# Kernel tuning notes

Measured on AMD Instinct MI355X. Metric: run time of the kernel, lower is better.

Reference implementation:

```python
import jax, jax.numpy as jnp
import numpy as np

N_NODES = 100000
N_EDGES = 600000
H = 128
NUM_STEPS = 5


def setup_inputs() -> dict:
    key = jax.random.key(0)
    ks = jax.random.split(key, 8)
    s = 0.05  # small init scale to keep gates in a sane range
    return {
        "x": jax.random.normal(ks[0], (N_NODES, H), dtype=jnp.float32),
        "edge_index": jax.random.randint(ks[1], (2, N_EDGES), 0, N_NODES, dtype=jnp.int64),
        "W_msg": jax.random.normal(ks[2], (H, H), dtype=jnp.float32) * s,
        "b_msg": jax.random.normal(ks[3], (H,), dtype=jnp.float32) * s,
        "W_ih": jax.random.normal(ks[4], (3 * H, H), dtype=jnp.float32) * s,
        "W_hh": jax.random.normal(ks[5], (3 * H, H), dtype=jnp.float32) * s,
        "b_ih": jax.random.normal(ks[6], (3 * H,), dtype=jnp.float32) * s,
        "b_hh": jax.random.normal(ks[7], (3 * H,), dtype=jnp.float32) * s,
    }


def reference(x, edge_index, W_msg, b_msg, W_ih, W_hh, b_ih, b_hh):
    num_nodes = x.shape[0]
    row, col = edge_index[0], edge_index[1]

    def step(h, _):
        # gather source features, transform, scatter-add to destinations
        messages = h[col] @ W_msg.T + b_msg                      # [E, H]
        agg = jax.ops.segment_sum(messages, row, num_segments=num_nodes)  # [N, H]
        # PyTorch GRUCell: gate order (r, z, n) in weight_ih/weight_hh
        gi = agg @ W_ih.T + b_ih                                  # [N, 3H]
        gh = h @ W_hh.T + b_hh                                    # [N, 3H]
        i_r, i_z, i_n = jnp.split(gi, 3, axis=-1)
        h_r, h_z, h_n = jnp.split(gh, 3, axis=-1)
        r = jax.nn.sigmoid(i_r + h_r)
        z = jax.nn.sigmoid(i_z + h_z)
        n = jnp.tanh(i_n + r * h_n)
        h_new = (1.0 - z) * n + z * h
        return h_new, None

    h, _ = jax.lax.scan(step, x, None, length=NUM_STEPS)
    return h
```

## Files before the change

### kernel.cpp

```cpp
#include <hip/hip_runtime.h>

#define N_NODESC 100000
#define N_EDGESC 600000
#define HDIM 128
#define H3 384
#define NUM_STEPSC 5

#define SCAN_BLOCK 256
#define SCAN_CHUNK 1024

typedef __attribute__((ext_vector_type(8))) short bf16x8;
typedef __attribute__((ext_vector_type(4))) float f32x4;

__device__ __forceinline__ unsigned short f2bf(float x) {
    union { float f; unsigned int u; } v; v.f = x;
    unsigned int r = v.u + 0x7FFF + ((v.u >> 16) & 1);
    return (unsigned short)(r >> 16);
}
__device__ __forceinline__ float bf2f(unsigned short lo16) {
    union { unsigned int u; float f; } v; v.u = (unsigned int)lo16 << 16; return v.f;
}

__device__ __forceinline__ float fast_sigmoid(float x) {
    float e = __builtin_amdgcn_exp2f(-1.44269504f * x);
    return __builtin_amdgcn_rcpf(1.0f + e);
}
__device__ __forceinline__ float fast_tanh(float x) {
    float e = __builtin_amdgcn_exp2f(2.88539008f * x);
    return 1.0f - 2.0f * __builtin_amdgcn_rcpf(1.0f + e);
}

__global__ void prep_pack(const float* __restrict__ W_msg, const float* __restrict__ b_msg,
                          const float* __restrict__ W_ih, const float* __restrict__ W_hh,
                          unsigned short* __restrict__ Wc, unsigned short* __restrict__ Wh,
                          float* __restrict__ b_c)
{
    int tid = blockIdx.x * blockDim.x + threadIdx.x;
    if (tid >= HDIM * H3) return;
    int j = tid % H3;
    int k = tid / H3;
    float wc = 0.f;
    for (int m = 0; m < HDIM; ++m)
        wc = fmaf(W_ih[j*HDIM + m], W_msg[m*HDIM + k], wc);
    float wh = W_hh[j*HDIM + k];
    int kt = k >> 5, kk = k & 31, jt = j >> 4, jj = j & 15;
    int lane = ((kk >> 3) << 4) + jj;
    int e = kk & 7;
    size_t idx = ((size_t)(kt*24 + jt)*64 + lane)*8 + e;
    Wc[idx] = f2bf(wc);
    Wh[idx] = f2bf(wh);
    if (k == 0) {
        float bb = 0.f;
        for (int m = 0; m < HDIM; ++m) bb = fmaf(W_ih[j*HDIM + m], b_msg[m], bb);
        b_c[j] = bb;
    }
}

__global__ void init_hbf(const float* __restrict__ x, unsigned short* __restrict__ h_bf)
{
    int i = blockIdx.x * blockDim.x + threadIdx.x;
    if (i >= N_NODESC * HDIM / 4) return;
    float4 v = ((const float4*)x)[i];
    ushort4 b;
    b.x = f2bf(v.x); b.y = f2bf(v.y); b.z = f2bf(v.z); b.w = f2bf(v.w);
    ((ushort4*)h_bf)[i] = b;
}

__global__ void hist_kernel(const int* __restrict__ eidx, int* __restrict__ deg)
{
    int e = blockIdx.x * blockDim.x + threadIdx.x;
    if (e < N_EDGESC) atomicAdd(&deg[eidx[e]], 1);
}

__global__ void scan_partial(const int* __restrict__ in, int* __restrict__ out,
                             int* __restrict__ bsums, int n)
{
    __shared__ int ts[SCAN_BLOCK];
    int tid = threadIdx.x;
    int base = blockIdx.x * SCAN_CHUNK + tid * 4;
    int v0 = (base+0 < n) ? in[base+0] : 0;
    int v1 = (base+1 < n) ? in[base+1] : 0;
    int v2 = (base+2 < n) ? in[base+2] : 0;
    int v3 = (base+3 < n) ? in[base+3] : 0;
    ts[tid] = v0+v1+v2+v3;
    __syncthreads();
    for (int off = 1; off < SCAN_BLOCK; off <<= 1) {
        int t = (tid >= off) ? ts[tid-off] : 0;
        __syncthreads();
        ts[tid] += t;
        __syncthreads();
    }
    int excl = (tid > 0) ? ts[tid-1] : 0;
    if (tid == SCAN_BLOCK-1) bsums[blockIdx.x] = ts[SCAN_BLOCK-1];
    if (base+0 < n) out[base+0] = excl;
    if (base+1 < n) out[base+1] = excl + v0;
    if (base+2 < n) out[base+2] = excl + v0 + v1;
    if (base+3 < n) out[base+3] = excl + v0 + v1 + v2;
}

__global__ void scan_sums(int* bsums, int nb)
{
    if (threadIdx.x == 0 && blockIdx.x == 0) {
        int run = 0;
        for (int b = 0; b < nb; ++b) { int t = bsums[b]; bsums[b] = run; run += t; }
    }
}

__global__ void scan_add(int* __restrict__ out, const int* __restrict__ bsums, int n,
                         int* __restrict__ cur)
{
    int i = blockIdx.x * blockDim.x + threadIdx.x;
    if (i < n) {
        int v = out[i] + bsums[i / SCAN_CHUNK];
        out[i] = v;
        if (i < N_NODESC) cur[i] = v;
    }
}

__global__ void scatter_edges(const int* __restrict__ eidx, int* __restrict__ cur,
                              int* __restrict__ cols)
{
    int e = blockIdx.x * blockDim.x + threadIdx.x;
    if (e < N_EDGESC) {
        int r = eidx[e];
        int c = eidx[N_EDGESC + e];
        int p = atomicAdd(&cur[r], 1);
        cols[p] = c;
    }
}

#define GRU_M 32
__global__ __launch_bounds__(512) void gnn_step(
    const unsigned short* __restrict__ hb_src, unsigned short* __restrict__ hb_dst,
    float* __restrict__ h_out,
    const int* __restrict__ offs, const int* __restrict__ cols,
    const unsigned short* __restrict__ Wc, const unsigned short* __restrict__ Wh,
    const float* __restrict__ b_c, const float* __restrict__ b_ih, const float* __restrict__ b_hh)
{
    __shared__ __align__(16) unsigned short LB[2 * GRU_M * HDIM];
    unsigned short* Sl = LB;
    unsigned short* Hl = LB + GRU_M * HDIM;
    __shared__ float Dl[GRU_M];

    int tid = threadIdx.x;
    int i0 = blockIdx.x * GRU_M;

    int srow = tid >> 4;
    int cb   = (tid & 15) << 4;
    int pb   = srow*256 + (cb ^ ((srow & 7) << 4));

    *(float4*)((char*)Hl + pb) =
        *(const float4*)((const char*)hb_src + (size_t)(i0 + srow)*256 + cb);

    int beg = offs[i0 + srow], end = offs[i0 + srow + 1];
    float acc[8] = {0.f,0.f,0.f,0.f,0.f,0.f,0.f,0.f};
    int e = beg;
    for (; e + 3 < end; e += 4) {
        int s0 = cols[e+0], s1 = cols[e+1], s2 = cols[e+2], s3 = cols[e+3];
        bf16x8 v0 = *(const bf16x8*)((const char*)hb_src + (size_t)s0*256 + cb);
        bf16x8 v1 = *(const bf16x8*)((const char*)hb_src + (size_t)s1*256 + cb);
        bf16x8 v2 = *(const bf16x8*)((const char*)hb_src + (size_t)s2*256 + cb);
        bf16x8 v3 = *(const bf16x8*)((const char*)hb_src + (size_t)s3*256 + cb);
        #pragma unroll
        for (int j = 0; j < 8; ++j) {
            float t0 = bf2f((unsigned short)v0[j]) + bf2f((unsigned short)v1[j]);
            float t1 = bf2f((unsigned short)v2[j]) + bf2f((unsigned short)v3[j]);
            acc[j] += t0 + t1;
        }
    }
    if (e + 1 < end) {
        int s0 = cols[e], s1 = cols[e+1];
        bf16x8 v0 = *(const bf16x8*)((const char*)hb_src + (size_t)s0*256 + cb);
        bf16x8 v1 = *(const bf16x8*)((const char*)hb_src + (size_t)s1*256 + cb);
        #pragma unroll
        for (int j = 0; j < 8; ++j)
            acc[j] += bf2f((unsigned short)v0[j]) + bf2f((unsigned short)v1[j]);
        e += 2;
    }
    if (e < end) {
        bf16x8 v0 = *(const bf16x8*)((const char*)hb_src + (size_t)cols[e]*256 + cb);
        #pragma unroll
        for (int j = 0; j < 8; ++j) acc[j] += bf2f((unsigned short)v0[j]);
    }
    union { ushort2 u2[4]; float4 f4; } pk;
    #pragma unroll
    for (int j = 0; j < 4; ++j) {
        pk.u2[j].x = f2bf(acc[2*j]);
        pk.u2[j].y = f2bf(acc[2*j+1]);
    }
    *(float4*)((char*)Sl + pb) = pk.f4;
    if ((tid & 15) == 0) Dl[srow] = (float)(end - beg);
    __syncthreads();

    int lane = tid & 63;
    int wid  = tid >> 6;
    int kg   = lane >> 4;
    int lr   = lane & 15;
    int c    = (wid << 4) + lr;

    f32x4 a_cr[2], a_cz[2], a_cn[2], a_hr[2], a_hz[2], a_hn[2];
    #pragma unroll
    for (int t = 0; t < 2; ++t) {
        a_cr[t] = (f32x4){0,0,0,0}; a_cz[t] = (f32x4){0,0,0,0}; a_cn[t] = (f32x4){0,0,0,0};
        a_hr[t] = (f32x4){0,0,0,0}; a_hz[t] = (f32x4){0,0,0,0}; a_hn[t] = (f32x4){0,0,0,0};
    }

    int r0 = lr, r1 = 16 + lr;
    int x0 = (r0 & 7) << 4, x1 = (r1 & 7) << 4;

    #pragma unroll
    for (int kc = 0; kc < 4; ++kc) {
        int cbk = kc*64 + kg*16;
        bf16x8 aS0 = *(const bf16x8*)((const char*)Sl + r0*256 + (cbk ^ x0));
        bf16x8 aS1 = *(const bf16x8*)((const char*)Sl + r1*256 + (cbk ^ x1));
        bf16x8 aH0 = *(const bf16x8*)((const char*)Hl + r0*256 + (cbk ^ x0));
        bf16x8 aH1 = *(const bf16x8*)((const char*)Hl + r1*256 + (cbk ^ x1));
        const bf16x8* Bc = (const bf16x8*)Wc + (size_t)kc*1536 + lane;
        const bf16x8* Bh = (const bf16x8*)Wh + (size_t)kc*1536 + lane;
        bf16x8 b;
        b = Bc[(size_t)(wid     ) * 64];
        a_cr[0] = __builtin_amdgcn_mfma_f32_16x16x32_bf16(aS0, b, a_cr[0], 0, 0, 0);
        a_cr[1] = __builtin_amdgcn_mfma_f32_16x16x32_bf16(aS1, b, a_cr[1], 0, 0, 0);
        b = Bc[(size_t)(wid +  8) * 64];
        a_cz[0] = __builtin_amdgcn_mfma_f32_16x16x32_bf16(aS0, b, a_cz[0], 0, 0, 0);
        a_cz[1] = __builtin_amdgcn_mfma_f32_16x16x32_bf16(aS1, b, a_cz[1], 0, 0, 0);
        b = Bc[(size_t)(wid + 16) * 64];
        a_cn[0] = __builtin_amdgcn_mfma_f32_16x16x32_bf16(aS0, b, a_cn[0], 0, 0, 0);
        a_cn[1] = __builtin_amdgcn_mfma_f32_16x16x32_bf16(aS1, b, a_cn[1], 0, 0, 0);
        b = Bh[(size_t)(wid     ) * 64];
        a_hr[0] = __builtin_amdgcn_mfma_f32_16x16x32_bf16(aH0, b, a_hr[0], 0, 0, 0);
        a_hr[1] = __builtin_amdgcn_mfma_f32_16x16x32_bf16(aH1, b, a_hr[1], 0, 0, 0);
        b = Bh[(size_t)(wid +  8) * 64];
        a_hz[0] = __builtin_amdgcn_mfma_f32_16x16x32_bf16(aH0, b, a_hz[0], 0, 0, 0);
        a_hz[1] = __builtin_amdgcn_mfma_f32_16x16x32_bf16(aH1, b, a_hz[1], 0, 0, 0);
        b = Bh[(size_t)(wid + 16) * 64];
        a_hn[0] = __builtin_amdgcn_mfma_f32_16x16x32_bf16(aH0, b, a_hn[0], 0, 0, 0);
        a_hn[1] = __builtin_amdgcn_mfma_f32_16x16x32_bf16(aH1, b, a_hn[1], 0, 0, 0);
    }

    float bc_r = b_c[c],  bc_z = b_c[c+128],  bc_n = b_c[c+256];
    float bs_r = b_ih[c]     + b_hh[c];
    float bs_z = b_ih[c+128] + b_hh[c+128];
    float bi_n = b_ih[c+256], bh_n = b_hh[c+256];

    float hv[2][4];
    #pragma unroll
    for (int t = 0; t < 2; ++t) {
        #pragma unroll
        for (int q = 0; q < 4; ++q) {
            int row = t*16 + (kg << 2) + q;
            float dg = Dl[row];
            float r  = fast_sigmoid(a_cr[t][q] + a_hr[t][q] + fmaf(dg, bc_r, bs_r));
            float z  = fast_sigmoid(a_cz[t][q] + a_hz[t][q] + fmaf(dg, bc_z, bs_z));
            float gin = a_cn[t][q] + fmaf(dg, bc_n, bi_n);
            float ghn = a_hn[t][q] + bh_n;
            float nn = fast_tanh(fmaf(r, ghn, gin));
            float hold = bf2f(*(const unsigned short*)((const char*)Hl + row*256 + ((c*2) ^ ((row & 7) << 4))));
            hv[t][q] = fmaf(z, hold - nn, nn);
        }
    }
    __syncthreads();

    if (!h_out) {
        #pragma unroll
        for (int t = 0; t < 2; ++t)
            #pragma unroll
            for (int q = 0; q < 4; ++q) {
                int row = t*16 + (kg << 2) + q;
                *(unsigned short*)((char*)Sl + row*256 + ((c*2) ^ ((row & 7) << 4))) = f2bf(hv[t][q]);
            }
        __syncthreads();
        *(float4*)((char*)hb_dst + (size_t)(i0 + srow)*256 + cb) =
            *(const float4*)((const char*)Sl + pb);
    } else {
        float* F = (float*)LB;
        #pragma unroll
        for (int t = 0; t < 2; ++t)
            #pragma unroll
            for (int q = 0; q < 4; ++q) {
                int row = t*16 + (kg << 2) + q;
                *(float*)((char*)F + row*512 + ((c*4) ^ ((row & 7) << 4))) = hv[t][q];
            }
        __syncthreads();
        int sr2 = tid >> 5;
        int cb2 = (tid & 31) << 4;
        #pragma unroll
        for (int half = 0; half < 2; ++half) {
            int rr = half*16 + sr2;
            float4 v = *(const float4*)((const char*)F + rr*512 + (cb2 ^ ((rr & 7) << 4)));
            *(float4*)((char*)h_out + (size_t)(i0 + rr)*512 + cb2) = v;
        }
    }
}

extern "C" void kernel_launch(void* const* d_in, const int* in_sizes, int n_in,
                              void* d_out, int out_size, void* d_ws, size_t ws_size,
                              hipStream_t stream)
{
    const float* x     = (const float*)d_in[0];
    const int*   eidx  = (const int*)d_in[1];
    const float* W_msg = (const float*)d_in[2];
    const float* b_msg = (const float*)d_in[3];
    const float* W_ih  = (const float*)d_in[4];
    const float* W_hh  = (const float*)d_in[5];
    const float* b_ih  = (const float*)d_in[6];
    const float* b_hh  = (const float*)d_in[7];

    float* h = (float*)d_out;

    char* ws = (char*)d_ws;
    size_t off = 0;
    auto alloc = [&](size_t bytes) -> void* {
        void* p = ws + off;
        off = (off + bytes + 255) & ~(size_t)255;
        return p;
    };
    unsigned short* hb0 = (unsigned short*)alloc((size_t)N_NODESC*HDIM*sizeof(unsigned short));
    unsigned short* hb1 = (unsigned short*)alloc((size_t)N_NODESC*HDIM*sizeof(unsigned short));
    unsigned short* Wc  = (unsigned short*)alloc((size_t)HDIM*H3*sizeof(unsigned short));
    unsigned short* Wh  = (unsigned short*)alloc((size_t)HDIM*H3*sizeof(unsigned short));
    float* b_c    = (float*)alloc(H3*sizeof(float));
    int*   deg    = (int*)alloc((N_NODESC+1)*sizeof(int));
    int*   offs   = (int*)alloc((N_NODESC+1)*sizeof(int));
    int*   cur    = (int*)alloc(N_NODESC*sizeof(int));
    int*   cols   = (int*)alloc(N_EDGESC*sizeof(int));
    int*   bsums  = (int*)alloc(256*sizeof(int));

    hipMemsetAsync(deg, 0, (N_NODESC+1)*sizeof(int), stream);

    init_hbf<<<(N_NODESC*HDIM/4 + 255)/256, 256, 0, stream>>>(x, hb0);
    prep_pack<<<(HDIM*H3 + 255)/256, 256, 0, stream>>>(W_msg, b_msg, W_ih, W_hh, Wc, Wh, b_c);

    hist_kernel<<<(N_EDGESC + 255)/256, 256, 0, stream>>>(eidx, deg);

    int n_scan = N_NODESC + 1;
    int nb = (n_scan + SCAN_CHUNK - 1) / SCAN_CHUNK;
    scan_partial<<<nb, SCAN_BLOCK, 0, stream>>>(deg, offs, bsums, n_scan);
    scan_sums<<<1, 64, 0, stream>>>(bsums, nb);
    scan_add<<<(n_scan + 255)/256, 256, 0, stream>>>(offs, bsums, n_scan, cur);

    scatter_edges<<<(N_EDGESC + 255)/256, 256, 0, stream>>>(eidx, cur, cols);

    for (int step = 0; step < NUM_STEPSC; ++step) {
        const unsigned short* src = (step & 1) ? hb1 : hb0;
        unsigned short*       dst = (step & 1) ? hb0 : hb1;
        float* out = (step == NUM_STEPSC - 1) ? h : nullptr;
        gnn_step<<<N_NODESC/GRU_M, 512, 0, stream>>>(src, dst, out, offs, cols,
                                                     Wc, Wh, b_c, b_ih, b_hh);
    }
}
```

Baseline: 430.7 us.

## Make GRU step kernel persistent with weights held in registers

The per-step kernel now launches a fixed grid of 256 blocks that loop over the 3125 node tiles. Each block loads its packed weight fragments into registers once instead of reloading them per tile. Launch bounds are tightened to two blocks per CU. The risk is that 256 blocks of 512 threads may underfill the MI355X's CUs, and a persistent loop loses the latency hiding that many resident blocks give the irregular gather; register pressure also rises.

```diff
diff --git a/kernel.cpp b/kernel.cpp
--- a/kernel.cpp
+++ b/kernel.cpp
@@ -8,6 +8,10 @@
 
 #define SCAN_BLOCK 256
 #define SCAN_CHUNK 1024
+
+#define GRU_M 32
+#define NT_TILES (N_NODESC / GRU_M)
+#define PERSIST_GRID 256
 
 typedef __attribute__((ext_vector_type(8))) short bf16x8;
 typedef __attribute__((ext_vector_type(4))) float f32x4;
@@ -129,8 +133,7 @@
     }
 }
 
-#define GRU_M 32
-__global__ __launch_bounds__(512) void gnn_step(
+__global__ __launch_bounds__(512, 2) void gnn_step(
     const unsigned short* __restrict__ hb_src, unsigned short* __restrict__ hb_dst,
     float* __restrict__ h_out,
     const int* __restrict__ offs, const int* __restrict__ cols,
@@ -143,153 +146,162 @@
     __shared__ float Dl[GRU_M];
 
     int tid = threadIdx.x;
-    int i0 = blockIdx.x * GRU_M;
-
-    int srow = tid >> 4;
-    int cb   = (tid & 15) << 4;
-    int pb   = srow*256 + (cb ^ ((srow & 7) << 4));
-
-    *(float4*)((char*)Hl + pb) =
-        *(const float4*)((const char*)hb_src + (size_t)(i0 + srow)*256 + cb);
-
-    int beg = offs[i0 + srow], end = offs[i0 + srow + 1];
-    float acc[8] = {0.f,0.f,0.f,0.f,0.f,0.f,0.f,0.f};
-    int e = beg;
-    for (; e + 3 < end; e += 4) {
-        int s0 = cols[e+0], s1 = cols[e+1], s2 = cols[e+2], s3 = cols[e+3];
-        bf16x8 v0 = *(const bf16x8*)((const char*)hb_src + (size_t)s0*256 + cb);
-        bf16x8 v1 = *(const bf16x8*)((const char*)hb_src + (size_t)s1*256 + cb);
-        bf16x8 v2 = *(const bf16x8*)((const char*)hb_src + (size_t)s2*256 + cb);
-        bf16x8 v3 = *(const bf16x8*)((const char*)hb_src + (size_t)s3*256 + cb);
-        #pragma unroll
-        for (int j = 0; j < 8; ++j) {
-            float t0 = bf2f((unsigned short)v0[j]) + bf2f((unsigned short)v1[j]);
-            float t1 = bf2f((unsigned short)v2[j]) + bf2f((unsigned short)v3[j]);
-            acc[j] += t0 + t1;
-        }
-    }
-    if (e + 1 < end) {
-        int s0 = cols[e], s1 = cols[e+1];
-        bf16x8 v0 = *(const bf16x8*)((const char*)hb_src + (size_t)s0*256 + cb);
-        bf16x8 v1 = *(const bf16x8*)((const char*)hb_src + (size_t)s1*256 + cb);
-        #pragma unroll
-        for (int j = 0; j < 8; ++j)
-            acc[j] += bf2f((unsigned short)v0[j]) + bf2f((unsigned short)v1[j]);
-        e += 2;
-    }
-    if (e < end) {
-        bf16x8 v0 = *(const bf16x8*)((const char*)hb_src + (size_t)cols[e]*256 + cb);
-        #pragma unroll
-        for (int j = 0; j < 8; ++j) acc[j] += bf2f((unsigned short)v0[j]);
-    }
-    union { ushort2 u2[4]; float4 f4; } pk;
-    #pragma unroll
-    for (int j = 0; j < 4; ++j) {
-        pk.u2[j].x = f2bf(acc[2*j]);
-        pk.u2[j].y = f2bf(acc[2*j+1]);
-    }
-    *(float4*)((char*)Sl + pb) = pk.f4;
-    if ((tid & 15) == 0) Dl[srow] = (float)(end - beg);
-    __syncthreads();
-
     int lane = tid & 63;
     int wid  = tid >> 6;
     int kg   = lane >> 4;
     int lr   = lane & 15;
     int c    = (wid << 4) + lr;
 
-    f32x4 a_cr[2], a_cz[2], a_cn[2], a_hr[2], a_hz[2], a_hn[2];
-    #pragma unroll
-    for (int t = 0; t < 2; ++t) {
-        a_cr[t] = (f32x4){0,0,0,0}; a_cz[t] = (f32x4){0,0,0,0}; a_cn[t] = (f32x4){0,0,0,0};
-        a_hr[t] = (f32x4){0,0,0,0}; a_hz[t] = (f32x4){0,0,0,0}; a_hn[t] = (f32x4){0,0,0,0};
-    }
-
-    int r0 = lr, r1 = 16 + lr;
-    int x0 = (r0 & 7) << 4, x1 = (r1 & 7) << 4;
-
-    #pragma unroll
-    for (int kc = 0; kc < 4; ++kc) {
-        int cbk = kc*64 + kg*16;
-        bf16x8 aS0 = *(const bf16x8*)((const char*)Sl + r0*256 + (cbk ^ x0));
-        bf16x8 aS1 = *(const bf16x8*)((const char*)Sl + r1*256 + (cbk ^ x1));
-        bf16x8 aH0 = *(const bf16x8*)((const char*)Hl + r0*256 + (cbk ^ x0));
-        bf16x8 aH1 = *(const bf16x8*)((const char*)Hl + r1*256 + (cbk ^ x1));
-        const bf16x8* Bc = (const bf16x8*)Wc + (size_t)kc*1536 + lane;
-        const bf16x8* Bh = (const bf16x8*)Wh + (size_t)kc*1536 + lane;
-        bf16x8 b;
-        b = Bc[(size_t)(wid     ) * 64];
-        a_cr[0] = __builtin_amdgcn_mfma_f32_16x16x32_bf16(aS0, b, a_cr[0], 0, 0, 0);
-        a_cr[1] = __builtin_amdgcn_mfma_f32_16x16x32_bf16(aS1, b, a_cr[1], 0, 0, 0);
-        b = Bc[(size_t)(wid +  8) * 64];
-        a_cz[0] = __builtin_amdgcn_mfma_f32_16x16x32_bf16(aS0, b, a_cz[0], 0, 0, 0);
-        a_cz[1] = __builtin_amdgcn_mfma_f32_16x16x32_bf16(aS1, b, a_cz[1], 0, 0, 0);
-        b = Bc[(size_t)(wid + 16) * 64];
-        a_cn[0] = __builtin_amdgcn_mfma_f32_16x16x32_bf16(aS0, b, a_cn[0], 0, 0, 0);
-        a_cn[1] = __builtin_amdgcn_mfma_f32_16x16x32_bf16(aS1, b, a_cn[1], 0, 0, 0);
-        b = Bh[(size_t)(wid     ) * 64];
-        a_hr[0] = __builtin_amdgcn_mfma_f32_16x16x32_bf16(aH0, b, a_hr[0], 0, 0, 0);
-        a_hr[1] = __builtin_amdgcn_mfma_f32_16x16x32_bf16(aH1, b, a_hr[1], 0, 0, 0);
-        b = Bh[(size_t)(wid +  8) * 64];
-        a_hz[0] = __builtin_amdgcn_mfma_f32_16x16x32_bf16(aH0, b, a_hz[0], 0, 0, 0);
-        a_hz[1] = __builtin_amdgcn_mfma_f32_16x16x32_bf16(aH1, b, a_hz[1], 0, 0, 0);
-        b = Bh[(size_t)(wid + 16) * 64];
-        a_hn[0] = __builtin_amdgcn_mfma_f32_16x16x32_bf16(aH0, b, a_hn[0], 0, 0, 0);
-        a_hn[1] = __builtin_amdgcn_mfma_f32_16x16x32_bf16(aH1, b, a_hn[1], 0, 0, 0);
-    }
+    int srow = tid >> 4;
+    int cb   = (tid & 15) << 4;
+    int pb   = srow*256 + (cb ^ ((srow & 7) << 4));
 
     float bc_r = b_c[c],  bc_z = b_c[c+128],  bc_n = b_c[c+256];
     float bs_r = b_ih[c]     + b_hh[c];
     float bs_z = b_ih[c+128] + b_hh[c+128];
     float bi_n = b_ih[c+256], bh_n = b_hh[c+256];
 
-    float hv[2][4];
+    bf16x8 wcr[4], wcz[4], wcn[4], whr[4], whz[4], whn[4];
     #pragma unroll
-    for (int t = 0; t < 2; ++t) {
+    for (int kc = 0; kc < 4; ++kc) {
+        const bf16x8* Bc = (const bf16x8*)Wc + (size_t)kc*1536 + lane;
+        const bf16x8* Bh = (const bf16x8*)Wh + (size_t)kc*1536 + lane;
+        wcr[kc] = Bc[(size_t)(wid     ) * 64];
+        wcz[kc] = Bc[(size_t)(wid +  8) * 64];
+        wcn[kc] = Bc[(size_t)(wid + 16) * 64];
+        whr[kc] = Bh[(size_t)(wid     ) * 64];
+        whz[kc] = Bh[(size_t)(wid +  8) * 64];
+        whn[kc] = Bh[(size_t)(wid + 16) * 64];
+    }
+
+    int r0 = lr, r1 = 16 + lr;
+    int x0 = (r0 & 7) << 4, x1 = (r1 & 7) << 4;
+
+    for (int tile = blockIdx.x; tile < NT_TILES; tile += PERSIST_GRID) {
+        int i0 = tile * GRU_M;
+
+        *(float4*)((char*)Hl + pb) =
+            *(const float4*)((const char*)hb_src + (size_t)(i0 + srow)*256 + cb);
+
+        int beg = offs[i0 + srow], end = offs[i0 + srow + 1];
+        float acc[8] = {0.f,0.f,0.f,0.f,0.f,0.f,0.f,0.f};
+        int e = beg;
+        for (; e + 3 < end; e += 4) {
+            int s0 = cols[e+0], s1 = cols[e+1], s2 = cols[e+2], s3 = cols[e+3];
+            bf16x8 v0 = *(const bf16x8*)((const char*)hb_src + (size_t)s0*256 + cb);
+            bf16x8 v1 = *(const bf16x8*)((const char*)hb_src + (size_t)s1*256 + cb);
+            bf16x8 v2 = *(const bf16x8*)((const char*)hb_src + (size_t)s2*256 + cb);
+            bf16x8 v3 = *(const bf16x8*)((const char*)hb_src + (size_t)s3*256 + cb);
+            #pragma unroll
+            for (int j = 0; j < 8; ++j) {
+                float t0 = bf2f((unsigned short)v0[j]) + bf2f((unsigned short)v1[j]);
+                float t1 = bf2f((unsigned short)v2[j]) + bf2f((unsigned short)v3[j]);
+                acc[j] += t0 + t1;
+            }
+        }
+        if (e + 1 < end) {
+            int s0 = cols[e], s1 = cols[e+1];
+            bf16x8 v0 = *(const bf16x8*)((const char*)hb_src + (size_t)s0*256 + cb);
+            bf16x8 v1 = *(const bf16x8*)((const char*)hb_src + (size_t)s1*256 + cb);
+            #pragma unroll
+            for (int j = 0; j < 8; ++j)
+                acc[j] += bf2f((unsigned short)v0[j]) + bf2f((unsigned short)v1[j]);
+            e += 2;
+        }
+        if (e < end) {
+            bf16x8 v0 = *(const bf16x8*)((const char*)hb_src + (size_t)cols[e]*256 + cb);
+            #pragma unroll
+            for (int j = 0; j < 8; ++j) acc[j] += bf2f((unsigned short)v0[j]);
+        }
+        {
+            union { ushort2 u2[4]; float4 f4; } pk;
+            #pragma unroll
+            for (int j = 0; j < 4; ++j) {
+                pk.u2[j].x = f2bf(acc[2*j]);
+                pk.u2[j].y = f2bf(acc[2*j+1]);
+            }
+            *(float4*)((char*)Sl + pb) = pk.f4;
+        }
+        if ((tid & 15) == 0) Dl[srow] = (float)(end - beg);
+        __syncthreads();
+
+        f32x4 a_cr[2], a_cz[2], a_cn[2], a_hr[2], a_hz[2], a_hn[2];
         #pragma unroll
-        for (int q = 0; q < 4; ++q) {
-            int row = t*16 + (kg << 2) + q;
-            float dg = Dl[row];
-            float r  = fast_sigmoid(a_cr[t][q] + a_hr[t][q] + fmaf(dg, bc_r, bs_r));
-            float z  = fast_sigmoid(a_cz[t][q] + a_hz[t][q] + fmaf(dg, bc_z, bs_z));
-            float gin = a_cn[t][q] + fmaf(dg, bc_n, bi_n);
-            float ghn = a_hn[t][q] + bh_n;
-            float nn = fast_tanh(fmaf(r, ghn, gin));
-            float hold = bf2f(*(const unsigned short*)((const char*)Hl + row*256 + ((c*2) ^ ((row & 7) << 4))));
-            hv[t][q] = fmaf(z, hold - nn, nn);
-        }
-    }
-    __syncthreads();
-
-    if (!h_out) {
+        for (int t = 0; t < 2; ++t) {
+            a_cr[t] = (f32x4){0,0,0,0}; a_cz[t] = (f32x4){0,0,0,0}; a_cn[t] = (f32x4){0,0,0,0};
+            a_hr[t] = (f32x4){0,0,0,0}; a_hz[t] = (f32x4){0,0,0,0}; a_hn[t] = (f32x4){0,0,0,0};
+        }
+
         #pragma unroll
-        for (int t = 0; t < 2; ++t)
+        for (int kc = 0; kc < 4; ++kc) {
+            int cbk = kc*64 + kg*16;
+            bf16x8 aS0 = *(const bf16x8*)((const char*)Sl + r0*256 + (cbk ^ x0));
+            bf16x8 aS1 = *(const bf16x8*)((const char*)Sl + r1*256 + (cbk ^ x1));
+            bf16x8 aH0 = *(const bf16x8*)((const char*)Hl + r0*256 + (cbk ^ x0));
+            bf16x8 aH1 = *(const bf16x8*)((const char*)Hl + r1*256 + (cbk ^ x1));
+            a_cr[0] = __builtin_amdgcn_mfma_f32_16x16x32_bf16(aS0, wcr[kc], a_cr[0], 0, 0, 0);
+            a_cr[1] = __builtin_amdgcn_mfma_f32_16x16x32_bf16(aS1, wcr[kc], a_cr[1], 0, 0, 0);
+            a_cz[0] = __builtin_amdgcn_mfma_f32_16x16x32_bf16(aS0, wcz[kc], a_cz[0], 0, 0, 0);
+            a_cz[1] = __builtin_amdgcn_mfma_f32_16x16x32_bf16(aS1, wcz[kc], a_cz[1], 0, 0, 0);
+            a_cn[0] = __builtin_amdgcn_mfma_f32_16x16x32_bf16(aS0, wcn[kc], a_cn[0], 0, 0, 0);
+            a_cn[1] = __builtin_amdgcn_mfma_f32_16x16x32_bf16(aS1, wcn[kc], a_cn[1], 0, 0, 0);
+            a_hr[0] = __builtin_amdgcn_mfma_f32_16x16x32_bf16(aH0, whr[kc], a_hr[0], 0, 0, 0);
+            a_hr[1] = __builtin_amdgcn_mfma_f32_16x16x32_bf16(aH1, whr[kc], a_hr[1], 0, 0, 0);
+            a_hz[0] = __builtin_amdgcn_mfma_f32_16x16x32_bf16(aH0, whz[kc], a_hz[0], 0, 0, 0);
+            a_hz[1] = __builtin_amdgcn_mfma_f32_16x16x32_bf16(aH1, whz[kc], a_hz[1], 0, 0, 0);
+            a_hn[0] = __builtin_amdgcn_mfma_f32_16x16x32_bf16(aH0, whn[kc], a_hn[0], 0, 0, 0);
+            a_hn[1] = __builtin_amdgcn_mfma_f32_16x16x32_bf16(aH1, whn[kc], a_hn[1], 0, 0, 0);
+        }
+
+        float hv[2][4];
+        #pragma unroll
+        for (int t = 0; t < 2; ++t) {
             #pragma unroll
             for (int q = 0; q < 4; ++q) {
                 int row = t*16 + (kg << 2) + q;
-                *(unsigned short*)((char*)Sl + row*256 + ((c*2) ^ ((row & 7) << 4))) = f2bf(hv[t][q]);
+                float dg = Dl[row];
+                float r  = fast_sigmoid(a_cr[t][q] + a_hr[t][q] + fmaf(dg, bc_r, bs_r));
+                float z  = fast_sigmoid(a_cz[t][q] + a_hz[t][q] + fmaf(dg, bc_z, bs_z));
+                float gin = a_cn[t][q] + fmaf(dg, bc_n, bi_n);
+                float ghn = a_hn[t][q] + bh_n;
+                float nn = fast_tanh(fmaf(r, ghn, gin));
+                float hold = bf2f(*(const unsigned short*)((const char*)Hl + row*256 + ((c*2) ^ ((row & 7) << 4))));
+                hv[t][q] = fmaf(z, hold - nn, nn);
             }
-        __syncthreads();
-        *(float4*)((char*)hb_dst + (size_t)(i0 + srow)*256 + cb) =
-            *(const float4*)((const char*)Sl + pb);
-    } else {
-        float* F = (float*)LB;
-        #pragma unroll
-        for (int t = 0; t < 2; ++t)
-            #pragma unroll
-            for (int q = 0; q < 4; ++q) {
-                int row = t*16 + (kg << 2) + q;
-                *(float*)((char*)F + row*512 + ((c*4) ^ ((row & 7) << 4))) = hv[t][q];
+        }
+        __syncthreads();
+
+        if (!h_out) {
+            #pragma unroll
+            for (int t = 0; t < 2; ++t)
+                #pragma unroll
+                for (int q = 0; q < 4; ++q) {
+                    int row = t*16 + (kg << 2) + q;
+                    *(unsigned short*)((char*)Sl + row*256 + ((c*2) ^ ((row & 7) << 4))) = f2bf(hv[t][q]);
+                }
+            __syncthreads();
+            *(float4*)((char*)hb_dst + (size_t)(i0 + srow)*256 + cb) =
+                *(const float4*)((const char*)Sl + pb);
+        } else {
+            float* F = (float*)LB;
+            #pragma unroll
+            for (int t = 0; t < 2; ++t)
+                #pragma unroll
+                for (int q = 0; q < 4; ++q) {
+                    int row = t*16 + (kg << 2) + q;
+                    *(float*)((char*)F + row*512 + ((c*4) ^ ((row & 7) << 4))) = hv[t][q];
+                }
+            __syncthreads();
+            int sr2 = tid >> 5;
+            int cb2 = (tid & 31) << 4;
+            #pragma unroll
+            for (int half = 0; half < 2; ++half) {
+                int rr = half*16 + sr2;
+                float4 v = *(const float4*)((const char*)F + rr*512 + (cb2 ^ ((rr & 7) << 4)));
+                *(float4*)((char*)h_out + (size_t)(i0 + rr)*512 + cb2) = v;
             }
-        __syncthreads();
-        int sr2 = tid >> 5;
-        int cb2 = (tid & 31) << 4;
-        #pragma unroll
-        for (int half = 0; half < 2; ++half) {
-            int rr = half*16 + sr2;
-            float4 v = *(const float4*)((const char*)F + rr*512 + (cb2 ^ ((rr & 7) << 4)));
-            *(float4*)((char*)h_out + (size_t)(i0 + rr)*512 + cb2) = v;
-        }
+        }
+        __syncthreads();
     }
 }
 
@@ -345,7 +357,7 @@
         const unsigned short* src = (step & 1) ? hb1 : hb0;
         unsigned short*       dst = (step & 1) ? hb0 : hb1;
         float* out = (step == NUM_STEPSC - 1) ? h : nullptr;
-        gnn_step<<<N_NODESC/GRU_M, 512, 0, stream>>>(src, dst, out, offs, cols,
-                                                     Wc, Wh, b_c, b_ih, b_hh);
-    }
-}
+        gnn_step<<<PERSIST_GRID, 512, 0, stream>>>(src, dst, out, offs, cols,
+                                                   Wc, Wh, b_c, b_ih, b_hh);
+    }
+}
```

Result: slower. 517.7 us (+20.2%).
